# Kernel optimization log

Hardware: AMD Instinct MI355X
Metric: run time of the kernel (lower is better)

The kernel has to match this reference:

```python
import jax, jax.numpy as jnp
import numpy as np
from jax import lax

EPS = 1e-6


def _layernorm(x, g, b, eps=1e-5):
    m = x.mean(-1, keepdims=True)
    v = x.var(-1, keepdims=True)
    return (x - m) / jnp.sqrt(v + eps) * g + b


def _causal_conv(x, w, b, dilation):
    # x: [B,S,D], w: [K, D_in, D_out] -> causal (left) padded dilated conv + GELU, residual
    k = w.shape[0]
    pad = (k - 1) * dilation
    y = lax.conv_general_dilated(
        x, w, window_strides=(1,), padding=[(pad, 0)], rhs_dilation=(dilation,),
        dimension_numbers=('NWC', 'WIO', 'NWC'))
    return x + jax.nn.gelu(y + b)


def setup_inputs() -> dict:
    key = jax.random.key(0)
    B, S, D, DC, N_LTM, K_WM, KS = 4, 2048, 1024, 256, 768, 8, 5
    ks = jax.random.split(key, 24)
    sc = 0.02

    def n(k, shape, scale=sc):
        return jax.random.normal(k, shape, jnp.float32) * scale

    return {
        'x': jax.random.normal(ks[0], (B, S, D), jnp.float32),
        'cache': jax.random.normal(ks[1], (B, N_LTM, DC), jnp.float32),
        'wm': jax.random.normal(ks[2], (B, K_WM, DC + 1), jnp.float32),
        # LTM read projections
        'Wq_ltm': n(ks[3], (D, DC)), 'Wo_ltm': n(ks[4], (DC, D)), 'wg_ltm': n(ks[5], (D,)),
        # WM read projections
        'Wq_wm': n(ks[6], (D, DC)), 'Wo_wm': n(ks[7], (DC, D)), 'wg_wm': n(ks[8], (D,)),
        # causal dilated conv stack (2 layers, k=5, dilations 1 and 2)
        'conv1_w': n(ks[9], (KS, D, D)), 'conv1_b': jnp.zeros((D,), jnp.float32),
        'conv2_w': n(ks[10], (KS, D, D)), 'conv2_b': jnp.zeros((D,), jnp.float32),
        'ln_g': jnp.ones((D,), jnp.float32), 'ln_b': jnp.zeros((D,), jnp.float32),
        # WM write (learned slot keys for addressing)
        'Wqw_wm': n(ks[11], (D, DC)), 'Ww_wm': n(ks[12], (D, DC)),
        'wm_keys': n(ks[13], (K_WM, DC), 1.0), 'wgw_wm': n(ks[14], (D,)),
        # LTM write (content-based addressing against cache)
        'Wqw_ltm': n(ks[15], (D, DC)), 'Ww_ltm': n(ks[16], (D, DC)), 'wgw_ltm': n(ks[17], (D,)),
    }


def reference(x, cache, wm, Wq_ltm, Wo_ltm, wg_ltm, Wq_wm, Wo_wm, wg_wm,
              conv1_w, conv1_b, conv2_w, conv2_b, ln_g, ln_b,
              Wqw_wm, Ww_wm, wm_keys, wgw_wm, Wqw_ltm, Ww_ltm, wgw_ltm):
    DC = cache.shape[-1]
    inv_sqrt = 1.0 / jnp.sqrt(jnp.float32(DC))

    # ---- LTM READ: content-addressed soft read, gated residual blend ----
    q = x @ Wq_ltm                                                  # [B,S,DC]
    attn = jax.nn.softmax(jnp.einsum('bsd,bnd->bsn', q, cache) * inv_sqrt, -1)
    read = jnp.einsum('bsn,bnd->bsd', attn, cache)                  # [B,S,DC]
    gate = jax.nn.sigmoid(x @ wg_ltm)[..., None]                    # [B,S,1]
    x_ltm = x + gate * (read @ Wo_ltm)

    # ---- WM READ (read_decay=0.0 -> wm unchanged by read) ----
    content = wm[..., :DC]                                          # [B,Kw,DC]
    q2 = x_ltm @ Wq_wm
    attn2 = jax.nn.softmax(jnp.einsum('bsd,bkd->bsk', q2, content) * inv_sqrt, -1)
    read2 = jnp.einsum('bsk,bkd->bsd', attn2, content)
    gate2 = jax.nn.sigmoid(x_ltm @ wg_wm)[..., None]
    x_enh = x_ltm + gate2 * (read2 @ Wo_wm)

    # ---- COMPUTE: causal dilated conv stack + post-LayerNorm ----
    h = _causal_conv(x_enh, conv1_w, conv1_b, 1)
    h = _causal_conv(h, conv2_w, conv2_b, 2)
    out = _layernorm(h, ln_g, ln_b)                                 # [B,S,D]

    # ---- WM WRITE: gated soft-WTA addressing vs learned slot keys ----
    qw = out @ Wqw_wm                                               # [B,S,DC]
    aw = jax.nn.softmax(jnp.einsum('bsd,kd->bsk', qw, wm_keys) * inv_sqrt, -1)
    gw = jax.nn.sigmoid(out @ wgw_wm)[..., None]                    # [B,S,1]
    w = gw * aw                                                     # [B,S,Kw]
    tot = w.sum(1)                                                  # [B,Kw]
    c = out @ Ww_wm                                                 # [B,S,DC]
    avg = jnp.einsum('bsk,bsd->bkd', w, c) / (tot[..., None] + EPS)
    alpha = jnp.clip(tot, 0.0, 1.0)[..., None]
    new_content = (1.0 - alpha) * content + alpha * avg
    new_valid = jnp.clip(wm[..., DC] + tot, 0.0, 1.0)               # validity channel
    updated_wm = jnp.concatenate([new_content, new_valid[..., None]], -1)

    # ---- LTM WRITE: gated soft blended write, content-addressed vs cache ----
    ql = out @ Wqw_ltm
    al = jax.nn.softmax(jnp.einsum('bsd,bnd->bsn', ql, cache) * inv_sqrt, -1)
    gl = jax.nn.sigmoid(out @ wgw_ltm)[..., None]
    wl = gl * al                                                    # [B,S,N]
    totl = wl.sum(1)                                                # [B,N]
    cl = out @ Ww_ltm
    avgl = jnp.einsum('bsn,bsd->bnd', wl, cl) / (totl[..., None] + EPS)
    alphal = jnp.clip(totl, 0.0, 1.0)[..., None]
    updated_cache = (1.0 - alphal) * cache + alphal * avgl

    return (out, updated_cache, updated_wm)
```

## Files before the change

### kernel.cpp

```cpp
#include <hip/hip_runtime.h>
#include <stdint.h>

typedef unsigned short u16;
typedef unsigned int u32;
typedef __attribute__((ext_vector_type(8))) short s16x8;
typedef __attribute__((ext_vector_type(4))) float f32x4;

__device__ __forceinline__ float bf2f(u16 u) {
    return __builtin_bit_cast(float, (u32)u << 16);
}
__device__ __forceinline__ u16 f2bf(float f) {
    u32 u = __builtin_bit_cast(u32, f);
    u += 0x7FFFu + ((u >> 16) & 1u);
    return (u16)(u >> 16);
}

__device__ __forceinline__ void gl16(const u16* g, u16* l) {
    __builtin_amdgcn_global_load_lds(
        (const __attribute__((address_space(1))) u32*)(const void*)g,
        (__attribute__((address_space(3))) u32*)(void*)l, 16, 0, 0);
}

#define BAR() { __builtin_amdgcn_sched_barrier(0); __builtin_amdgcn_s_barrier(); __builtin_amdgcn_sched_barrier(0); }

template<int DIL>
__global__ __launch_bounds__(512) void conv8_k(
    const u16* __restrict__ Apad, const u16* __restrict__ Bw,
    float* __restrict__ Cf, float* __restrict__ Cf2)
{
    __shared__ u16 sA[2][16384];
    __shared__ u16 sB[2][16384];
    const int tid  = threadIdx.x;
    const int wid  = tid >> 6;
    const int lane = tid & 63;
    const int wr = (wid >> 2) * 128;
    const int wc = (wid & 3) * 64;
    const int lr = lane & 15;
    const int kq = lane >> 4;
    const int batch = blockIdx.x >> 3;
    const int m0b   = (blockIdx.x & 7) * 256;
    const int bn0   = blockIdx.y * 256;
    const int kbeg  = blockIdx.z * 2560;
    const u16* Ab = Apad + (long)batch * 2056 * 1024;

    const int row0 = tid >> 3;
    const int g0   = (tid & 7) ^ (row0 & 7);

    f32x4 acc[8][4] = {};
    s16x8 aF[4][2], bF[4][2];

    auto stageA = [&](int nb, int kt, int h) {
        const int ktabs = kbeg + kt * 64;
        const int tap = ktabs >> 10;
        const long rbase = (long)(8 + m0b + h * 128 + (tap - 4) * DIL) * 1024
                           + (ktabs & 1023) + g0 * 8;
        u16* dst = &sA[nb][h * 8192 + tid * 8];
        gl16(Ab + rbase + (long)row0 * 1024, dst);
        gl16(Ab + rbase + (long)(row0 + 64) * 1024, dst + 4096);
    };
    auto stageB = [&](int nb, int kt, int h) {
        const int ktabs = kbeg + kt * 64;
        const long rbase = (long)(bn0 + h * 128) * 5120 + ktabs + g0 * 8;
        u16* dst = &sB[nb][h * 8192 + tid * 8];
        gl16(Bw + rbase + (long)row0 * 5120, dst);
        gl16(Bw + rbase + (long)(row0 + 64) * 5120, dst + 4096);
    };
    auto readA = [&](int nb, int mq) {
        #pragma unroll
        for (int m = 0; m < 4; m++) {
            const int row = wr + (mq * 4 + m) * 16 + lr;
            #pragma unroll
            for (int ks = 0; ks < 2; ks++) {
                const int chunk = ks * 4 + kq;
                aF[m][ks] = *(const s16x8*)&sA[nb][row * 64 + ((chunk ^ (row & 7)) << 3)];
            }
        }
    };
    auto readB4 = [&](int nb, int nq) {
        #pragma unroll
        for (int n = 0; n < 2; n++) {
            const int row = wc + (nq * 2 + n) * 16 + lr;
            #pragma unroll
            for (int ks = 0; ks < 2; ks++) {
                const int chunk = ks * 4 + kq;
                bF[nq * 2 + n][ks] = *(const s16x8*)&sB[nb][row * 64 + ((chunk ^ (row & 7)) << 3)];
            }
        }
    };

#define MFQ(MQ, NQ) \
    { __builtin_amdgcn_s_setprio(1); \
      _Pragma("unroll") \
      for (int m = 0; m < 4; m++) { \
        _Pragma("unroll") \
        for (int n = 0; n < 2; n++) { \
          _Pragma("unroll") \
          for (int ks = 0; ks < 2; ks++) \
            acc[(MQ)*4+m][(NQ)*2+n] = __builtin_amdgcn_mfma_f32_16x16x32_bf16( \
                aF[m][ks], bF[(NQ)*2+n][ks], acc[(MQ)*4+m][(NQ)*2+n], 0, 0, 0); \
        } } \
      __builtin_amdgcn_s_setprio(0); }

    stageB(0, 0, 0); stageB(0, 0, 1); stageA(0, 0, 0); stageA(0, 0, 1);

    const int NT = 40;
    for (int t = 0; t < NT; ++t) {
        const int nb = t & 1;
        asm volatile("s_waitcnt vmcnt(4)" ::: "memory");
        BAR();
        readB4(nb, 0); readB4(nb, 1);
        if (t + 1 < NT) { stageB(nb ^ 1, t + 1, 0); stageB(nb ^ 1, t + 1, 1); }
        if (t + 1 < NT) { asm volatile("s_waitcnt vmcnt(4)" ::: "memory"); }
        else            { asm volatile("s_waitcnt vmcnt(0)" ::: "memory"); }
        BAR();
        readA(nb, 0);
        MFQ(0, 0); MFQ(0, 1);
        if (t + 1 < NT) { stageA(nb ^ 1, t + 1, 0); stageA(nb ^ 1, t + 1, 1); }
        readA(nb, 1);
        MFQ(1, 0); MFQ(1, 1);
    }
#undef MFQ

    float* C = (blockIdx.z ? Cf2 : Cf) + (long)batch * 2048 * 1024;
    #pragma unroll
    for (int m = 0; m < 8; m++) {
        #pragma unroll
        for (int n = 0; n < 4; n++) {
            const int cc = bn0 + wc + n * 16 + lr;
            #pragma unroll
            for (int j = 0; j < 4; j++) {
                const int r = m0b + wr + m * 16 + kq * 4 + j;
                C[(long)r * 1024 + cc] = acc[m][n][j];
            }
        }
    }
}

template<int AL, int BL, int EPI, int TN, int KS, int SWZ>
__global__ __launch_bounds__(256) void gemm_bf16(
    const u16* __restrict__ A, const u16* __restrict__ B,
    float* __restrict__ Cf, u16* __restrict__ Cb,
    const float* __restrict__ res, const float* __restrict__ gate,
    int M, int N, int K, int lda, int ldb,
    long aBS, long bBS, long cBS,
    float* __restrict__ Pp, long pStride, int nby)
{
    constexpr int NFRAG = TN / 32;
    __shared__ u16 sA[128 * 32];
    __shared__ u16 sB[TN * 32];
    const int tid  = threadIdx.x;
    const int lane = tid & 63;
    const int wave = tid >> 6;
    const int wr = (wave >> 1) * 64;
    const int wc = (wave & 1) * (TN / 2);

    int bidx, bidy;
    if (SWZ) {
        const int nb  = gridDim.x;
        const int cpx = nb >> 3;
        const int bf  = blockIdx.x;
        const int sw  = (bf & 7) * cpx + (bf >> 3);
        bidx = sw / nby; bidy = sw - bidx * nby;
    } else {
        bidx = blockIdx.x; bidy = blockIdx.y;
    }
    const int m0 = bidx * 128;
    const int n0 = bidy * TN;
    const int zz = blockIdx.z;
    const long bz = (KS > 1) ? (zz / KS) : zz;
    const int ks  = (KS > 1) ? (zz % KS) : 0;
    const u16* Ab = A + bz * aBS;
    const u16* Bb = B + bz * bBS;

    f32x4 acc[4][NFRAG] = {};
    const int lr = lane & 15;
    const int lk = (lane >> 4) << 3;
    const int ar0 = tid >> 2;
    const int akg = (tid & 3) << 3;

    const int Kp = K / KS;
    const int kbeg = ks * Kp, kend = kbeg + Kp;

    for (int kk = kbeg; kk < kend; kk += 32) {
        __syncthreads();
        if (AL == 0) {
            gl16(Ab + (long)(m0 + ar0) * lda + kk + akg,      sA + tid * 8);
            gl16(Ab + (long)(m0 + ar0 + 64) * lda + kk + akg, sA + tid * 8 + 2048);
        } else {
            for (int t = tid; t < 512; t += 256) {
                int row = t & 127, kg = (t >> 7) << 3;
                u32 w0[4];
                #pragma unroll
                for (int j2 = 0; j2 < 4; j2++) {
                    u16 lo = Ab[(long)(kk + kg + 2*j2    ) * lda + m0 + row];
                    u16 hi = Ab[(long)(kk + kg + 2*j2 + 1) * lda + m0 + row];
                    w0[j2] = (u32)lo | ((u32)hi << 16);
                }
                uint4 v; v.x = w0[0]; v.y = w0[1]; v.z = w0[2]; v.w = w0[3];
                *reinterpret_cast<uint4*>(sA + row * 32 + kg) = v;
            }
        }
        if (BL == 1) {
            gl16(Bb + (long)(n0 + ar0) * ldb + kk + akg, sB + tid * 8);
            if (TN == 128)
                gl16(Bb + (long)(n0 + ar0 + 64) * ldb + kk + akg, sB + tid * 8 + 2048);
        } else {
            for (int t = tid; t < TN * 4; t += 256) {
                int col = t & (TN - 1), kg = (t / TN) << 3;
                u32 w0[4];
                #pragma unroll
                for (int j2 = 0; j2 < 4; j2++) {
                    u16 lo = Bb[(long)(kk + kg + 2*j2    ) * ldb + n0 + col];
                    u16 hi = Bb[(long)(kk + kg + 2*j2 + 1) * ldb + n0 + col];
                    w0[j2] = (u32)lo | ((u32)hi << 16);
                }
                uint4 v; v.x = w0[0]; v.y = w0[1]; v.z = w0[2]; v.w = w0[3];
                *reinterpret_cast<uint4*>(sB + col * 32 + kg) = v;
            }
        }
        __syncthreads();
        s16x8 aF[4], bF[NFRAG];
        #pragma unroll
        for (int m = 0; m < 4; m++)
            aF[m] = *reinterpret_cast<const s16x8*>(sA + (wr + m*16 + lr) * 32 + lk);
        #pragma unroll
        for (int n = 0; n < NFRAG; n++)
            bF[n] = *reinterpret_cast<const s16x8*>(sB + (wc + n*16 + lr) * 32 + lk);
        #pragma unroll
        for (int m = 0; m < 4; m++)
            #pragma unroll
            for (int n = 0; n < NFRAG; n++)
                acc[m][n] = __builtin_amdgcn_mfma_f32_16x16x32_bf16(aF[m], bF[n], acc[m][n], 0, 0, 0);
    }

    const int rj = (lane >> 4) << 2;
    if (KS > 1) {
        float* Pb = Pp + (long)ks * pStride + bz * cBS;
        #pragma unroll
        for (int m = 0; m < 4; m++)
            #pragma unroll
            for (int n = 0; n < NFRAG; n++) {
                const int cc = n0 + wc + n*16 + lr;
                #pragma unroll
                for (int j = 0; j < 4; j++) {
                    const int r = m0 + wr + m*16 + rj + j;
                    Pb[(long)r * N + cc] = acc[m][n][j];
                }
            }
        return;
    }

    float* Cfb = Cf + bz * cBS;
    #pragma unroll
    for (int m = 0; m < 4; m++) {
        #pragma unroll
        for (int n = 0; n < NFRAG; n++) {
            const int cc = n0 + wc + n*16 + lr;
            #pragma unroll
            for (int j = 0; j < 4; j++) {
                const int r = m0 + wr + m*16 + rj + j;
                const long idx = (long)r * N + cc;
                const float v = acc[m][n][j];
                if (EPI == 0) {
                    Cb[bz * cBS + idx] = f2bf(v);
                } else if (EPI == 1) {
                    Cfb[idx] = v;
                } else {
                    float o = res[idx] + gate[r] * v;
                    Cfb[idx] = o;
                    if (EPI == 2) Cb[idx] = f2bf(o);
                }
            }
        }
    }
}

template<int KS, int BF>
__global__ __launch_bounds__(256) void ksum_k(
    const float* __restrict__ Pp, long pStride,
    float* __restrict__ outf, u16* __restrict__ outb, int n4)
{
    int i = blockIdx.x * 256 + threadIdx.x;
    if (i >= n4) return;
    float4 s = reinterpret_cast<const float4*>(Pp)[i];
    #pragma unroll
    for (int k = 1; k < KS; k++) {
        float4 v = reinterpret_cast<const float4*>(Pp + (long)k * pStride)[i];
        s.x += v.x; s.y += v.y; s.z += v.z; s.w += v.w;
    }
    if (BF) {
        u32 lo = (u32)f2bf(s.x) | ((u32)f2bf(s.y) << 16);
        u32 hi = (u32)f2bf(s.z) | ((u32)f2bf(s.w) << 16);
        reinterpret_cast<uint2*>(outb)[i] = make_uint2(lo, hi);
    } else {
        reinterpret_cast<float4*>(outf)[i] = s;
    }
}

__global__ void zero_init_k(u16* __restrict__ a, u16* __restrict__ b,
                            float* __restrict__ tot, float* __restrict__ totl)
{
    int i = blockIdx.x * 256 + threadIdx.x;
    int bt = i >> 12, j = i & 4095;
    long off = (long)bt * (2056L * 1024 / 2) + j;
    reinterpret_cast<u32*>(a)[off] = 0u;
    reinterpret_cast<u32*>(b)[off] = 0u;
    if (i < 32) tot[i] = 0.f;
    if (i < 3072) totl[i] = 0.f;
}

__global__ void f32_to_bf16_k(const float* __restrict__ in, u16* __restrict__ out, int n4)
{
    int i = blockIdx.x * 256 + threadIdx.x;
    if (i < n4) {
        float4 v = reinterpret_cast<const float4*>(in)[i];
        u32 lo = (u32)f2bf(v.x) | ((u32)f2bf(v.y) << 16);
        u32 hi = (u32)f2bf(v.z) | ((u32)f2bf(v.w) << 16);
        reinterpret_cast<uint2*>(out)[i] = make_uint2(lo, hi);
    }
}

__global__ __launch_bounds__(256) void transpose_f32_bf16(
    const float* __restrict__ in, u16* __restrict__ out, int R, int C)
{
    __shared__ float tile[32][33];
    long zo = (long)blockIdx.z * R * C;
    in += zo; out += zo;
    int c0 = blockIdx.x * 32, r0 = blockIdx.y * 32;
    int tx = threadIdx.x & 31, ty = threadIdx.x >> 5;
    #pragma unroll
    for (int i = 0; i < 32; i += 8)
        tile[ty + i][tx] = in[(long)(r0 + ty + i) * C + c0 + tx];
    __syncthreads();
    #pragma unroll
    for (int i = 0; i < 32; i += 8)
        out[(long)(c0 + ty + i) * R + r0 + tx] = f2bf(tile[tx][ty + i]);
}

__global__ __launch_bounds__(256) void cw_k(
    const float* __restrict__ wm, const float* __restrict__ Wo, float* __restrict__ CW)
{
    int blk = blockIdx.x;
    const float* wrow = wm + (long)(blk >> 3) * 2056 + (blk & 7) * 257;
    int c = threadIdx.x;
    float a0 = 0.f, a1 = 0.f, a2 = 0.f, a3 = 0.f;
    for (int dd = 0; dd < 256; dd++) {
        float w = wrow[dd];
        const float* wo = Wo + (long)dd * 1024;
        a0 += w * wo[c]; a1 += w * wo[c + 256];
        a2 += w * wo[c + 512]; a3 += w * wo[c + 768];
    }
    float* o = CW + (long)blk * 1024;
    o[c] = a0; o[c + 256] = a1; o[c + 512] = a2; o[c + 768] = a3;
}

__global__ __launch_bounds__(256) void wc_k(
    const float* __restrict__ wm, const u16* __restrict__ WqWt, float* __restrict__ WC)
{
    int blk = blockIdx.x;
    const float* wrow = wm + (long)(blk >> 3) * 2056 + (blk & 7) * 257;
    int c = threadIdx.x;
    float a0 = 0.f, a1 = 0.f, a2 = 0.f, a3 = 0.f;
    for (int j = 0; j < 256; j++) {
        float w = wrow[j];
        const u16* wq = WqWt + (long)j * 1024;
        a0 += bf2f(wq[c])       * w;
        a1 += bf2f(wq[c + 256]) * w;
        a2 += bf2f(wq[c + 512]) * w;
        a3 += bf2f(wq[c + 768]) * w;
    }
    float* o = WC + (long)blk * 1024;
    o[c] = a0; o[c + 256] = a1; o[c + 512] = a2; o[c + 768] = a3;
}

__global__ __launch_bounds__(256) void gemv_sigmoid_k(
    const float* __restrict__ X, const float* __restrict__ w,
    float* __restrict__ out)
{
    int row  = blockIdx.x * 4 + (threadIdx.x >> 6);
    int lane = threadIdx.x & 63;
    const float* xr = X + (long)row * 1024;
    float s = 0.f;
    for (int i = lane; i < 1024; i += 64) s += xr[i] * w[i];
    #pragma unroll
    for (int o = 32; o > 0; o >>= 1) s += __shfl_down(s, o);
    if (lane == 0) out[row] = 1.f / (1.f + __expf(-s));
}

__global__ __launch_bounds__(256) void gemv_sigmoid2_k(
    const float* __restrict__ X, const float* __restrict__ w1, const float* __restrict__ w2,
    float* __restrict__ o1, float* __restrict__ o2)
{
    int row  = blockIdx.x * 4 + (threadIdx.x >> 6);
    int lane = threadIdx.x & 63;
    const float* xr = X + (long)row * 1024;
    float s1 = 0.f, s2 = 0.f;
    for (int i = lane; i < 1024; i += 64) {
        float xv = xr[i];
        s1 += xv * w1[i]; s2 += xv * w2[i];
    }
    #pragma unroll
    for (int o = 32; o > 0; o >>= 1) { s1 += __shfl_down(s1, o); s2 += __shfl_down(s2, o); }
    if (lane == 0) {
        o1[row] = 1.f / (1.f + __expf(-s1));
        o2[row] = 1.f / (1.f + __expf(-s2));
    }
}

__global__ __launch_bounds__(256) void softmax768_k(
    const float* __restrict__ scores, u16* __restrict__ out,
    const float* __restrict__ gate)
{
    __shared__ float s4[4], s4b[4];
    int row = blockIdx.x;
    int t = threadIdx.x;
    const float* sr = scores + (long)row * 768;
    float v[3];
    float m = -1e30f;
    #pragma unroll
    for (int i = 0; i < 3; i++) { v[i] = sr[t + i*256] * 0.0625f; m = fmaxf(m, v[i]); }
    float wm_ = m;
    #pragma unroll
    for (int o = 32; o > 0; o >>= 1) wm_ = fmaxf(wm_, __shfl_down(wm_, o));
    if ((t & 63) == 0) s4[t >> 6] = wm_;
    __syncthreads();
    float bm = fmaxf(fmaxf(s4[0], s4[1]), fmaxf(s4[2], s4[3]));
    float sum = 0.f;
    #pragma unroll
    for (int i = 0; i < 3; i++) { v[i] = __expf(v[i] - bm); sum += v[i]; }
    #pragma unroll
    for (int o = 32; o > 0; o >>= 1) sum += __shfl_down(sum, o);
    if ((t & 63) == 0) s4b[t >> 6] = sum;
    __syncthreads();
    float bs = s4b[0] + s4b[1] + s4b[2] + s4b[3];
    float g = gate ? gate[row] : 1.0f;
    float inv = g / bs;
    u16* orow = out + (long)row * 768;
    #pragma unroll
    for (int i = 0; i < 3; i++) orow[t + i*256] = f2bf(v[i] * inv);
}

__global__ __launch_bounds__(256) void wm_read_fused_k(
    const float* __restrict__ WC, const float* __restrict__ CW,
    const float* __restrict__ gate, const float* __restrict__ res,
    float* __restrict__ outf, u16* __restrict__ outb)
{
    __shared__ float sred[8][4];
    __shared__ float sa[8];
    int row = blockIdx.x;
    int b = row >> 11;
    int d = threadIdx.x, lane = d & 63, wave = d >> 6;
    long orow = (long)row * 1024;
    float rv0 = res[orow + d];
    float rv1 = res[orow + d + 256];
    float rv2 = res[orow + d + 512];
    float rv3 = res[orow + d + 768];
    const float* wcb = WC + (long)b * 8192;
    #pragma unroll
    for (int k = 0; k < 8; k++) {
        const float* w = wcb + k * 1024;
        float v = rv0 * w[d] + rv1 * w[d + 256] + rv2 * w[d + 512] + rv3 * w[d + 768];
        #pragma unroll
        for (int o = 32; o > 0; o >>= 1) v += __shfl_down(v, o);
        if (lane == 0) sred[k][wave] = v;
    }
    __syncthreads();
    if (d < 8) sa[d] = (sred[d][0] + sred[d][1] + sred[d][2] + sred[d][3]) * 0.0625f;
    __syncthreads();
    float m = sa[0];
    #pragma unroll
    for (int k = 1; k < 8; k++) m = fmaxf(m, sa[k]);
    float e[8], sum = 0.f;
    #pragma unroll
    for (int k = 0; k < 8; k++) { e[k] = __expf(sa[k] - m); sum += e[k]; }
    float inv = 1.f / sum;
    #pragma unroll
    for (int k = 0; k < 8; k++) e[k] *= inv;
    float g = gate[row];
    const float* cwb = CW + (long)b * 8192;
    long prow = ((long)(row >> 11) * 2056 + 8 + (row & 2047)) * 1024;
    float rv[4] = { rv0, rv1, rv2, rv3 };
    #pragma unroll
    for (int j = 0; j < 4; j++) {
        int c = d + j * 256;
        float acc = 0.f;
        #pragma unroll
        for (int k = 0; k < 8; k++) acc += e[k] * cwb[k * 1024 + c];
        float o = rv[j] + g * acc;
        outf[orow + c] = o;
        outb[prow + c] = f2bf(o);
    }
}

template<int PAD>
__global__ __launch_bounds__(256) void gelu_reduce_k(
    const float4* p0, const float4* p1, const float4* res,
    const float* __restrict__ bias, float4* outf, u16* outb)
{
    int i4 = blockIdx.x * 256 + threadIdx.x;
    int r = i4 >> 8, c4 = (i4 & 255) << 2;
    float4 a = p0[i4], b = p1[i4], rr = res[i4];
    float4 bi = *reinterpret_cast<const float4*>(bias + c4);
    float o[4];
    float y0 = a.x + b.x + bi.x, y1 = a.y + b.y + bi.y;
    float y2 = a.z + b.z + bi.z, y3 = a.w + b.w + bi.w;
    const float C0 = 0.79788456080286535588f, C1 = 0.044715f;
    o[0] = rr.x + 0.5f * y0 * (1.f + tanhf(C0 * (y0 + C1 * y0 * y0 * y0)));
    o[1] = rr.y + 0.5f * y1 * (1.f + tanhf(C0 * (y1 + C1 * y1 * y1 * y1)));
    o[2] = rr.z + 0.5f * y2 * (1.f + tanhf(C0 * (y2 + C1 * y2 * y2 * y2)));
    o[3] = rr.w + 0.5f * y3 * (1.f + tanhf(C0 * (y3 + C1 * y3 * y3 * y3)));
    float4 ov; ov.x = o[0]; ov.y = o[1]; ov.z = o[2]; ov.w = o[3];
    outf[i4] = ov;
    if (PAD) {
        long prow = ((long)(r >> 11) * 2056 + 8 + (r & 2047)) * 1024 + c4;
        u32 lo = (u32)f2bf(o[0]) | ((u32)f2bf(o[1]) << 16);
        u32 hi = (u32)f2bf(o[2]) | ((u32)f2bf(o[3]) << 16);
        *reinterpret_cast<uint2*>(outb + prow) = make_uint2(lo, hi);
    }
}

__global__ __launch_bounds__(256) void gelu_ln_k(
    const float4* __restrict__ p0, const float4* __restrict__ p1,
    const float4* __restrict__ res, const float* __restrict__ bias,
    const float* __restrict__ g, const float* __restrict__ b,
    float* __restrict__ outf, u16* __restrict__ outb)
{
    __shared__ float rs[4], rss[4];
    int row = blockIdx.x, t = threadIdx.x;
    long i4 = (long)row * 256 + t;
    float4 a = p0[i4], pb = p1[i4], rr = res[i4];
    float4 bi = reinterpret_cast<const float4*>(bias)[t];
    const float C0 = 0.79788456080286535588f, C1 = 0.044715f;
    float y0 = a.x + pb.x + bi.x, y1 = a.y + pb.y + bi.y;
    float y2 = a.z + pb.z + bi.z, y3 = a.w + pb.w + bi.w;
    float o0 = rr.x + 0.5f * y0 * (1.f + tanhf(C0 * (y0 + C1 * y0 * y0 * y0)));
    float o1 = rr.y + 0.5f * y1 * (1.f + tanhf(C0 * (y1 + C1 * y1 * y1 * y1)));
    float o2 = rr.z + 0.5f * y2 * (1.f + tanhf(C0 * (y2 + C1 * y2 * y2 * y2)));
    float o3 = rr.w + 0.5f * y3 * (1.f + tanhf(C0 * (y3 + C1 * y3 * y3 * y3)));
    float s  = o0 + o1 + o2 + o3;
    float ss = o0*o0 + o1*o1 + o2*o2 + o3*o3;
    #pragma unroll
    for (int o = 32; o > 0; o >>= 1) { s += __shfl_down(s, o); ss += __shfl_down(ss, o); }
    if ((t & 63) == 0) { rs[t >> 6] = s; rss[t >> 6] = ss; }
    __syncthreads();
    float S = rs[0]+rs[1]+rs[2]+rs[3];
    float SS = rss[0]+rss[1]+rss[2]+rss[3];
    float mean = S * (1.f/1024.f);
    float var  = SS * (1.f/1024.f) - mean*mean;
    float rstd = rsqrtf(var + 1e-5f);
    float4 gg = reinterpret_cast<const float4*>(g)[t];
    float4 bv = reinterpret_cast<const float4*>(b)[t];
    float4 y;
    y.x = (o0-mean)*rstd*gg.x + bv.x;
    y.y = (o1-mean)*rstd*gg.y + bv.y;
    y.z = (o2-mean)*rstd*gg.z + bv.z;
    y.w = (o3-mean)*rstd*gg.w + bv.w;
    reinterpret_cast<float4*>(outf)[i4] = y;
    u32 lo = (u32)f2bf(y.x) | ((u32)f2bf(y.y) << 16);
    u32 hi = (u32)f2bf(y.z) | ((u32)f2bf(y.w) << 16);
    reinterpret_cast<uint2*>(outb)[i4] = make_uint2(lo, hi);
}

__global__ __launch_bounds__(256) void attn8_w_k(
    const u16* __restrict__ q, int ldq, const u16* __restrict__ keys,
    const float* __restrict__ gate, float* __restrict__ w_out)
{
    __shared__ float sred[8][4];
    __shared__ float sa[8];
    int row = blockIdx.x;
    int d = threadIdx.x, lane = d & 63, wave = d >> 6;
    float qv = bf2f(q[(long)row * ldq + d]);
    #pragma unroll
    for (int k = 0; k < 8; k++) {
        float v = qv * bf2f(keys[k * 256 + d]);
        #pragma unroll
        for (int o = 32; o > 0; o >>= 1) v += __shfl_down(v, o);
        if (lane == 0) sred[k][wave] = v;
    }
    __syncthreads();
    if (d < 8) sa[d] = (sred[d][0] + sred[d][1] + sred[d][2] + sred[d][3]) * 0.0625f;
    __syncthreads();
    if (d < 8) {
        float m = sa[0];
        #pragma unroll
        for (int k = 1; k < 8; k++) m = fmaxf(m, sa[k]);
        float e = __expf(sa[d] - m), sum = 0.f;
        #pragma unroll
        for (int k = 0; k < 8; k++) sum += __expf(sa[k] - m);
        w_out[(long)row * 8 + d] = gate[row] * e / sum;
    }
}

__global__ __launch_bounds__(256) void tot8_k(const float* __restrict__ wD, float* __restrict__ tot)
{
    __shared__ float s4[4];
    int b = blockIdx.y;
    int s = blockIdx.x * 256 + threadIdx.x;
    const float* p = wD + ((long)b * 2048 + s) * 8;
    float v[8];
    #pragma unroll
    for (int k = 0; k < 8; k++) v[k] = p[k];
    for (int k = 0; k < 8; k++) {
        float xv = v[k];
        #pragma unroll
        for (int o = 32; o > 0; o >>= 1) xv += __shfl_down(xv, o);
        if ((threadIdx.x & 63) == 0) s4[threadIdx.x >> 6] = xv;
        __syncthreads();
        if (threadIdx.x == 0) atomicAdd(&tot[b*8 + k], s4[0]+s4[1]+s4[2]+s4[3]);
        __syncthreads();
    }
}

__global__ __launch_bounds__(256) void wm_avg_partial_k(
    const float* __restrict__ wD, const u16* __restrict__ cw, float* __restrict__ part)
{
    int blk = blockIdx.x;
    int b = blk >> 6, k = (blk >> 3) & 7, ch = blk & 7;
    int d = threadIdx.x;
    const float* wp = wD + ((long)b * 2048 + ch * 256) * 8 + k;
    const u16*   cp = cw + ((long)b * 2048 + ch * 256) * 1024 + 256 + d;
    float acc = 0.f;
    for (int s = 0; s < 256; s++) acc += wp[s * 8] * bf2f(cp[(long)s * 1024]);
    part[(long)blk * 256 + d] = acc;
}

__global__ __launch_bounds__(256) void wm_final_k(
    const float* __restrict__ part, const float* __restrict__ wm,
    const float* __restrict__ tot, float* __restrict__ out)
{
    int bk = blockIdx.x;
    int d = threadIdx.x;
    float acc = 0.f;
    #pragma unroll
    for (int ch = 0; ch < 8; ch++) acc += part[((long)bk * 8 + ch) * 256 + d];
    float t = tot[bk];
    float alpha = fminf(fmaxf(t, 0.f), 1.f);
    float avg = acc / (t + 1e-6f);
    long base = (long)(bk >> 3) * 2056 + (bk & 7) * 257;
    out[base + d] = (1.f - alpha) * wm[base + d] + alpha * avg;
    if (d == 0) out[base + 256] = fminf(fmaxf(wm[base + 256] + t, 0.f), 1.f);
}

__global__ void colsum_wl_k(const u16* __restrict__ wl, float* __restrict__ totl)
{
    int b = blockIdx.z;
    int n = blockIdx.x * 256 + threadIdx.x;
    int s0 = blockIdx.y * 256;
    const u16* p = wl + ((long)b * 2048 + s0) * 768 + n;
    float acc = 0.f;
    for (int s = 0; s < 256; s++) acc += bf2f(p[(long)s * 768]);
    atomicAdd(&totl[b * 768 + n], acc);
}

__global__ void cache_blend_k(const float* __restrict__ cache, const float* __restrict__ Sg,
                              const float* __restrict__ totl, float* __restrict__ out)
{
    long i = (long)blockIdx.x * 256 + threadIdx.x;
    int bn = (int)(i >> 8);
    float t = totl[bn];
    float a = fminf(fmaxf(t, 0.f), 1.f);
    out[i] = (1.f - a) * cache[i] + a * (Sg[i] / (t + 1e-6f));
}

extern "C" void kernel_launch(void* const* d_in, const int* in_sizes, int n_in,
                              void* d_out, int out_size, void* d_ws, size_t ws_size,
                              hipStream_t stream)
{
    const int D = 1024, DC = 256, NL = 768;
    const long MS = 8192;
    const long SB = 2048;

    const float* x       = (const float*)d_in[0];
    const float* cache   = (const float*)d_in[1];
    const float* wm      = (const float*)d_in[2];
    const float* Wq_ltm  = (const float*)d_in[3];
    const float* Wo_ltm  = (const float*)d_in[4];
    const float* wg_ltm  = (const float*)d_in[5];
    const float* Wq_wm   = (const float*)d_in[6];
    const float* Wo_wm   = (const float*)d_in[7];
    const float* wg_wm   = (const float*)d_in[8];
    const float* conv1_w = (const float*)d_in[9];
    const float* conv1_b = (const float*)d_in[10];
    const float* conv2_w = (const float*)d_in[11];
    const float* conv2_b = (const float*)d_in[12];
    const float* ln_g    = (const float*)d_in[13];
    const float* ln_b    = (const float*)d_in[14];
    const float* Wqw_wm  = (const float*)d_in[15];
    const float* Ww_wm   = (const float*)d_in[16];
    const float* wm_keys = (const float*)d_in[17];
    const float* wgw_wm  = (const float*)d_in[18];
    const float* Wqw_ltm = (const float*)d_in[19];
    const float* Ww_ltm  = (const float*)d_in[20];
    const float* wgw_ltm = (const float*)d_in[21];

    float* out_f     = (float*)d_out;
    float* cache_out = out_f + 8388608;
    float* wm_out    = out_f + 8388608 + 786432;

    char* ws = (char*)d_ws;
    size_t off = 0;
    auto alloc = [&](size_t bytes) -> char* {
        char* p = ws + off;
        off = (off + bytes + 255) & ~(size_t)255;
        return p;
    };
    u16* WqLt    = (u16*)alloc((size_t)D*DC*2);
    u16* WoLt    = (u16*)alloc((size_t)D*DC*2);
    u16* WqWt    = (u16*)alloc((size_t)D*DC*2);
    u16* WbigT   = (u16*)alloc((size_t)D*D*2);
    u16* c1wt    = (u16*)alloc((size_t)5*D*D*2);
    u16* c2wt    = (u16*)alloc((size_t)5*D*D*2);
    u16* cache_b = (u16*)alloc((size_t)4*NL*DC*2);
    u16* cache_t = (u16*)alloc((size_t)4*NL*DC*2);
    u16* keys_b  = (u16*)alloc((size_t)8*DC*2);
    u16* act0    = (u16*)alloc((size_t)MS*D*2);
    u16* act1    = (u16*)alloc((size_t)MS*D*2);
    u16* xpad1   = (u16*)alloc((size_t)4*2056*1024*2);
    u16* xpad2   = (u16*)alloc((size_t)4*2056*1024*2);
    u16* qb      = (u16*)alloc((size_t)MS*DC*2);
    u16* attnb   = (u16*)alloc((size_t)MS*NL*2);
    u16* readb   = (u16*)alloc((size_t)MS*DC*2);
    float* fact0 = (float*)alloc((size_t)MS*D*4);
    float* fact1 = (float*)alloc((size_t)MS*D*4);
    float* P     = (float*)alloc((size_t)MS*D*4);
    float* CW    = (float*)alloc((size_t)4*8*D*4);
    float* WC    = (float*)alloc((size_t)4*8*D*4);
    float* gateb = (float*)alloc((size_t)MS*4);
    float* gateb2= (float*)alloc((size_t)MS*4);
    float* wD    = (float*)alloc((size_t)MS*8*4);
    float* tot   = (float*)alloc((size_t)4*8*4);
    float* totl  = (float*)alloc((size_t)4*NL*4);
    float* part  = (float*)alloc((size_t)256*256*4);
    float* avglS = (float*)alloc((size_t)4*NL*DC*4);
    float* scores = fact0;
    u16*   qbig   = act0;

    auto cv = [&](const float* in, u16* out, long n) {
        long n4 = n / 4;
        f32_to_bf16_k<<<dim3((unsigned)((n4 + 255) / 256)), 256, 0, stream>>>(in, out, (int)n4);
    };
    auto tr = [&](const float* in, u16* out, int R, int C, int Z) {
        transpose_f32_bf16<<<dim3(C/32, R/32, Z), 256, 0, stream>>>(in, out, R, C);
    };

    zero_init_k<<<64, 256, 0, stream>>>(xpad1, xpad2, tot, totl);
    cv(x, act0, MS * D);
    cv(cache, cache_b, (long)4 * NL * DC);
    cv(wm_keys, keys_b, 8 * DC);
    tr(Wq_ltm,  WqLt,  D, DC, 1);
    tr(Wo_ltm,  WoLt,  DC, D, 1);
    tr(Wq_wm,   WqWt,  D, DC, 1);
    tr(Wqw_wm,  WbigT + 0*256*1024, D, DC, 1);
    tr(Ww_wm,   WbigT + 1*256*1024, D, DC, 1);
    tr(Wqw_ltm, WbigT + 2*256*1024, D, DC, 1);
    tr(Ww_ltm,  WbigT + 3*256*1024, D, DC, 1);
    tr(conv1_w, c1wt, 5*D, D, 1);
    tr(conv2_w, c2wt, 5*D, D, 1);
    tr(cache,   cache_t, NL, DC, 4);
    cw_k<<<32, 256, 0, stream>>>(wm, Wo_wm, CW);
    wc_k<<<32, 256, 0, stream>>>(wm, WqWt, WC);

    gemm_bf16<0,1,0,64,4,1><<<dim3(256,1,4), 256, 0, stream>>>(
        act0, WqLt, nullptr, nullptr, nullptr, nullptr,
        8192,256,1024,1024,1024, 0,0,0, P, 2097152L, 4);
    ksum_k<4,1><<<2048, 256, 0, stream>>>(P, 2097152L, nullptr, qb, 524288);
    gemv_sigmoid_k<<<2048, 256, 0, stream>>>(x, wg_ltm, gateb);
    gemm_bf16<0,1,1,128,1,1><<<dim3(96,1,4), 256, 0, stream>>>(
        qb, cache_b, scores, nullptr, nullptr, nullptr,
        2048,768,256,256,256, SB*256, (long)NL*DC, SB*768, nullptr, 0, 6);
    softmax768_k<<<8192, 256, 0, stream>>>(scores, attnb, nullptr);
    gemm_bf16<0,1,0,64,2,1><<<dim3(64,1,8), 256, 0, stream>>>(
        attnb, cache_t, nullptr, nullptr, nullptr, nullptr,
        2048,256,768,768,768, SB*768, (long)NL*DC, SB*256, P, 2097152L, 4);
    ksum_k<2,1><<<2048, 256, 0, stream>>>(P, 2097152L, nullptr, readb, 524288);
    gemm_bf16<0,1,5,128,1,1><<<dim3(512,1,1), 256, 0, stream>>>(
        readb, WoLt, fact0, nullptr, x, gateb,
        8192,1024,256,256,256, 0,0,0, nullptr, 0, 8);

    gemv_sigmoid_k<<<2048, 256, 0, stream>>>(fact0, wg_wm, gateb);
    wm_read_fused_k<<<8192, 256, 0, stream>>>(WC, CW, gateb, fact0, fact1, xpad1);

    conv8_k<1><<<dim3(32,4,2), 512, 0, stream>>>(xpad1, c1wt, fact0, P);
    gelu_reduce_k<1><<<8192, 256, 0, stream>>>(
        (const float4*)fact0, (const float4*)P, (const float4*)fact1,
        conv1_b, (float4*)fact0, xpad2);
    conv8_k<2><<<dim3(32,4,2), 512, 0, stream>>>(xpad2, c2wt, fact1, P);
    gelu_ln_k<<<8192, 256, 0, stream>>>(
        (const float4*)fact1, (const float4*)P, (const float4*)fact0,
        conv2_b, ln_g, ln_b, out_f, act1);

    gemm_bf16<0,1,0,128,1,1><<<dim3(512,1,1), 256, 0, stream>>>(
        act1, WbigT, nullptr, qbig, nullptr, nullptr,
        8192,1024,1024,1024,1024, 0,0,0, nullptr, 0, 8);
    gemv_sigmoid2_k<<<2048, 256, 0, stream>>>(out_f, wgw_wm, wgw_ltm, gateb, gateb2);
    attn8_w_k<<<8192, 256, 0, stream>>>(qbig, 1024, keys_b, gateb, wD);
    tot8_k<<<dim3(8, 4), 256, 0, stream>>>(wD, tot);
    wm_avg_partial_k<<<256, 256, 0, stream>>>(wD, qbig, part);
    wm_final_k<<<32, 256, 0, stream>>>(part, wm, tot, wm_out);

    gemm_bf16<0,1,1,128,1,1><<<dim3(96,1,4), 256, 0, stream>>>(
        qbig + 512, cache_b, scores, nullptr, nullptr, nullptr,
        2048,768,256,1024,256, SB*1024, (long)NL*DC, SB*768, nullptr, 0, 6);
    softmax768_k<<<8192, 256, 0, stream>>>(scores, attnb, gateb2);
    colsum_wl_k<<<dim3(3, 8, 4), 256, 0, stream>>>(attnb, totl);
    gemm_bf16<1,0,1,64,4,0><<<dim3(6,4,16), 256, 0, stream>>>(
        attnb, qbig + 768, nullptr, nullptr, nullptr, nullptr,
        768,256,2048,768,1024, SB*768, SB*1024, 196608L, P, 786432L, 0);
    ksum_k<4,0><<<768, 256, 0, stream>>>(P, 786432L, avglS, nullptr, 196608);
    cache_blend_k<<<3072, 256, 0, stream>>>(cache, avglS, totl, cache_out);

    (void)in_sizes; (void)n_in; (void)out_size; (void)ws_size;
}
```

Before: 577.0 us.

## Store split-K partials in bf16, merge transposes, fuse gate gemvs, swizzle conv grid

Split-K partial buffers for the conv and GEMM kernels are now written and read as bf16 instead of fp32, which halves the partial-sum traffic. All weight and cache transposes move into one launch, and the sigmoid gate gemvs are folded into the WM read and WM attention kernels. The conv grid is flattened with a block swizzle meant to improve L2 locality. Rounding partials to bf16 before summing loses accuracy in the conv outputs and the sums.

```diff
diff --git a/kernel.cpp b/kernel.cpp
--- a/kernel.cpp
+++ b/kernel.cpp
@@ -14,6 +14,10 @@
     u += 0x7FFFu + ((u >> 16) & 1u);
     return (u16)(u >> 16);
 }
+__device__ __forceinline__ void unpk4(uint2 r, float* o) {
+    o[0] = bf2f((u16)(r.x & 0xffff)); o[1] = bf2f((u16)(r.x >> 16));
+    o[2] = bf2f((u16)(r.y & 0xffff)); o[3] = bf2f((u16)(r.y >> 16));
+}
 
 __device__ __forceinline__ void gl16(const u16* g, u16* l) {
     __builtin_amdgcn_global_load_lds(
@@ -26,7 +30,7 @@
 template<int DIL>
 __global__ __launch_bounds__(512) void conv8_k(
     const u16* __restrict__ Apad, const u16* __restrict__ Bw,
-    float* __restrict__ Cf, float* __restrict__ Cf2)
+    u16* __restrict__ Cb0, u16* __restrict__ Cb1)
 {
     __shared__ u16 sA[2][16384];
     __shared__ u16 sB[2][16384];
@@ -37,10 +41,13 @@
     const int wc = (wid & 3) * 64;
     const int lr = lane & 15;
     const int kq = lane >> 4;
-    const int batch = blockIdx.x >> 3;
-    const int m0b   = (blockIdx.x & 7) * 256;
-    const int bn0   = blockIdx.y * 256;
-    const int kbeg  = blockIdx.z * 2560;
+    const int sw = (blockIdx.x & 7) * 32 + (blockIdx.x >> 3);
+    const int z    = sw >> 7;
+    const int bn0  = ((sw >> 5) & 3) * 256;
+    const int xm   = sw & 31;
+    const int batch = xm >> 3;
+    const int m0b   = (xm & 7) * 256;
+    const int kbeg  = z * 2560;
     const u16* Ab = Apad + (long)batch * 2056 * 1024;
 
     const int row0 = tid >> 3;
@@ -121,7 +128,7 @@
     }
 #undef MFQ
 
-    float* C = (blockIdx.z ? Cf2 : Cf) + (long)batch * 2048 * 1024;
+    u16* C = (z ? Cb1 : Cb0) + (long)batch * 2048 * 1024;
     #pragma unroll
     for (int m = 0; m < 8; m++) {
         #pragma unroll
@@ -130,7 +137,7 @@
             #pragma unroll
             for (int j = 0; j < 4; j++) {
                 const int r = m0b + wr + m * 16 + kq * 4 + j;
-                C[(long)r * 1024 + cc] = acc[m][n][j];
+                C[(long)r * 1024 + cc] = f2bf(acc[m][n][j]);
             }
         }
     }
@@ -143,7 +150,7 @@
     const float* __restrict__ res, const float* __restrict__ gate,
     int M, int N, int K, int lda, int ldb,
     long aBS, long bBS, long cBS,
-    float* __restrict__ Pp, long pStride, int nby)
+    u16* __restrict__ Pp, long pStride, int nby)
 {
     constexpr int NFRAG = TN / 32;
     __shared__ u16 sA[128 * 32];
@@ -235,7 +242,7 @@
 
     const int rj = (lane >> 4) << 2;
     if (KS > 1) {
-        float* Pb = Pp + (long)ks * pStride + bz * cBS;
+        u16* Pb = Pp + (long)ks * pStride + bz * cBS;
         #pragma unroll
         for (int m = 0; m < 4; m++)
             #pragma unroll
@@ -244,7 +251,7 @@
                 #pragma unroll
                 for (int j = 0; j < 4; j++) {
                     const int r = m0 + wr + m*16 + rj + j;
-                    Pb[(long)r * N + cc] = acc[m][n][j];
+                    Pb[(long)r * N + cc] = f2bf(acc[m][n][j]);
                 }
             }
         return;
@@ -277,23 +284,25 @@
 
 template<int KS, int BF>
 __global__ __launch_bounds__(256) void ksum_k(
-    const float* __restrict__ Pp, long pStride,
+    const u16* __restrict__ Pp, long pStride,
     float* __restrict__ outf, u16* __restrict__ outb, int n4)
 {
     int i = blockIdx.x * 256 + threadIdx.x;
     if (i >= n4) return;
-    float4 s = reinterpret_cast<const float4*>(Pp)[i];
-    #pragma unroll
-    for (int k = 1; k < KS; k++) {
-        float4 v = reinterpret_cast<const float4*>(Pp + (long)k * pStride)[i];
-        s.x += v.x; s.y += v.y; s.z += v.z; s.w += v.w;
+    float s[4] = {0.f, 0.f, 0.f, 0.f};
+    #pragma unroll
+    for (int k = 0; k < KS; k++) {
+        uint2 r = reinterpret_cast<const uint2*>(Pp + (long)k * pStride)[i];
+        float v[4]; unpk4(r, v);
+        s[0] += v[0]; s[1] += v[1]; s[2] += v[2]; s[3] += v[3];
     }
     if (BF) {
-        u32 lo = (u32)f2bf(s.x) | ((u32)f2bf(s.y) << 16);
-        u32 hi = (u32)f2bf(s.z) | ((u32)f2bf(s.w) << 16);
+        u32 lo = (u32)f2bf(s[0]) | ((u32)f2bf(s[1]) << 16);
+        u32 hi = (u32)f2bf(s[2]) | ((u32)f2bf(s[3]) << 16);
         reinterpret_cast<uint2*>(outb)[i] = make_uint2(lo, hi);
     } else {
-        reinterpret_cast<float4*>(outf)[i] = s;
+        float4 o; o.x = s[0]; o.y = s[1]; o.z = s[2]; o.w = s[3];
+        reinterpret_cast<float4*>(outf)[i] = o;
     }
 }
 
@@ -320,13 +329,42 @@
     }
 }
 
-__global__ __launch_bounds__(256) void transpose_f32_bf16(
-    const float* __restrict__ in, u16* __restrict__ out, int R, int C)
-{
+__global__ __launch_bounds__(256) void tr_all_k(
+    const float* __restrict__ Wq_ltm, const float* __restrict__ Wq_wm,
+    const float* __restrict__ Wqw_wm, const float* __restrict__ Ww_wm,
+    const float* __restrict__ Wqw_ltm, const float* __restrict__ Ww_ltm,
+    const float* __restrict__ Wo_ltm, const float* __restrict__ conv1_w,
+    const float* __restrict__ conv2_w, const float* __restrict__ cache,
+    u16* __restrict__ WqLt, u16* __restrict__ WqWt, u16* __restrict__ WbigT,
+    u16* __restrict__ WoLt, u16* __restrict__ c1wt, u16* __restrict__ c2wt,
+    u16* __restrict__ cache_t)
+{
+    int b = blockIdx.x;
+    const float* in; u16* out; int R, C, l;
+    if (b < 1536) {
+        l = b & 255; R = 1024; C = 256;
+        int m = b >> 8;
+        if      (m == 0) { in = Wq_ltm;  out = WqLt; }
+        else if (m == 1) { in = Wq_wm;   out = WqWt; }
+        else if (m == 2) { in = Wqw_wm;  out = WbigT; }
+        else if (m == 3) { in = Ww_wm;   out = WbigT + 262144; }
+        else if (m == 4) { in = Wqw_ltm; out = WbigT + 524288; }
+        else             { in = Ww_ltm;  out = WbigT + 786432; }
+    } else if (b < 1792) {
+        l = b - 1536; in = Wo_ltm; out = WoLt; R = 256; C = 1024;
+    } else if (b < 6912) {
+        l = b - 1792; in = conv1_w; out = c1wt; R = 5120; C = 1024;
+    } else if (b < 12032) {
+        l = b - 6912; in = conv2_w; out = c2wt; R = 5120; C = 1024;
+    } else {
+        int lb = b - 12032;
+        int z = lb / 192; l = lb % 192;
+        in = cache + (long)z * 196608; out = cache_t + (long)z * 196608;
+        R = 768; C = 256;
+    }
+    const int ct = C >> 5;
+    const int c0 = (l % ct) * 32, r0 = (l / ct) * 32;
     __shared__ float tile[32][33];
-    long zo = (long)blockIdx.z * R * C;
-    in += zo; out += zo;
-    int c0 = blockIdx.x * 32, r0 = blockIdx.y * 32;
     int tx = threadIdx.x & 31, ty = threadIdx.x >> 5;
     #pragma unroll
     for (int i = 0; i < 32; i += 8)
@@ -387,26 +425,6 @@
     if (lane == 0) out[row] = 1.f / (1.f + __expf(-s));
 }
 
-__global__ __launch_bounds__(256) void gemv_sigmoid2_k(
-    const float* __restrict__ X, const float* __restrict__ w1, const float* __restrict__ w2,
-    float* __restrict__ o1, float* __restrict__ o2)
-{
-    int row  = blockIdx.x * 4 + (threadIdx.x >> 6);
-    int lane = threadIdx.x & 63;
-    const float* xr = X + (long)row * 1024;
-    float s1 = 0.f, s2 = 0.f;
-    for (int i = lane; i < 1024; i += 64) {
-        float xv = xr[i];
-        s1 += xv * w1[i]; s2 += xv * w2[i];
-    }
-    #pragma unroll
-    for (int o = 32; o > 0; o >>= 1) { s1 += __shfl_down(s1, o); s2 += __shfl_down(s2, o); }
-    if (lane == 0) {
-        o1[row] = 1.f / (1.f + __expf(-s1));
-        o2[row] = 1.f / (1.f + __expf(-s2));
-    }
-}
-
 __global__ __launch_bounds__(256) void softmax768_k(
     const float* __restrict__ scores, u16* __restrict__ out,
     const float* __restrict__ gate)
@@ -442,11 +460,13 @@
 
 __global__ __launch_bounds__(256) void wm_read_fused_k(
     const float* __restrict__ WC, const float* __restrict__ CW,
-    const float* __restrict__ gate, const float* __restrict__ res,
+    const float* __restrict__ wg, const float* __restrict__ res,
     float* __restrict__ outf, u16* __restrict__ outb)
 {
     __shared__ float sred[8][4];
+    __shared__ float sg4[4];
     __shared__ float sa[8];
+    __shared__ float gsh;
     int row = blockIdx.x;
     int b = row >> 11;
     int d = threadIdx.x, lane = d & 63, wave = d >> 6;
@@ -455,6 +475,10 @@
     float rv1 = res[orow + d + 256];
     float rv2 = res[orow + d + 512];
     float rv3 = res[orow + d + 768];
+    float gp = rv0 * wg[d] + rv1 * wg[d + 256] + rv2 * wg[d + 512] + rv3 * wg[d + 768];
+    #pragma unroll
+    for (int o = 32; o > 0; o >>= 1) gp += __shfl_down(gp, o);
+    if (lane == 0) sg4[wave] = gp;
     const float* wcb = WC + (long)b * 8192;
     #pragma unroll
     for (int k = 0; k < 8; k++) {
@@ -466,6 +490,7 @@
     }
     __syncthreads();
     if (d < 8) sa[d] = (sred[d][0] + sred[d][1] + sred[d][2] + sred[d][3]) * 0.0625f;
+    if (d == 0) gsh = 1.f / (1.f + __expf(-(sg4[0] + sg4[1] + sg4[2] + sg4[3])));
     __syncthreads();
     float m = sa[0];
     #pragma unroll
@@ -476,7 +501,7 @@
     float inv = 1.f / sum;
     #pragma unroll
     for (int k = 0; k < 8; k++) e[k] *= inv;
-    float g = gate[row];
+    float g = gsh;
     const float* cwb = CW + (long)b * 8192;
     long prow = ((long)(row >> 11) * 2056 + 8 + (row & 2047)) * 1024;
     float rv[4] = { rv0, rv1, rv2, rv3 };
@@ -494,16 +519,19 @@
 
 template<int PAD>
 __global__ __launch_bounds__(256) void gelu_reduce_k(
-    const float4* p0, const float4* p1, const float4* res,
-    const float* __restrict__ bias, float4* outf, u16* outb)
+    const u16* __restrict__ p0, const u16* __restrict__ p1, const float4* __restrict__ res,
+    const float* __restrict__ bias, float4* __restrict__ outf, u16* __restrict__ outb)
 {
     int i4 = blockIdx.x * 256 + threadIdx.x;
     int r = i4 >> 8, c4 = (i4 & 255) << 2;
-    float4 a = p0[i4], b = p1[i4], rr = res[i4];
+    float a[4], b[4];
+    unpk4(reinterpret_cast<const uint2*>(p0)[i4], a);
+    unpk4(reinterpret_cast<const uint2*>(p1)[i4], b);
+    float4 rr = res[i4];
     float4 bi = *reinterpret_cast<const float4*>(bias + c4);
     float o[4];
-    float y0 = a.x + b.x + bi.x, y1 = a.y + b.y + bi.y;
-    float y2 = a.z + b.z + bi.z, y3 = a.w + b.w + bi.w;
+    float y0 = a[0] + b[0] + bi.x, y1 = a[1] + b[1] + bi.y;
+    float y2 = a[2] + b[2] + bi.z, y3 = a[3] + b[3] + bi.w;
     const float C0 = 0.79788456080286535588f, C1 = 0.044715f;
     o[0] = rr.x + 0.5f * y0 * (1.f + tanhf(C0 * (y0 + C1 * y0 * y0 * y0)));
     o[1] = rr.y + 0.5f * y1 * (1.f + tanhf(C0 * (y1 + C1 * y1 * y1 * y1)));
@@ -520,7 +548,7 @@
 }
 
 __global__ __launch_bounds__(256) void gelu_ln_k(
-    const float4* __restrict__ p0, const float4* __restrict__ p1,
+    const u16* __restrict__ p0, const u16* __restrict__ p1,
     const float4* __restrict__ res, const float* __restrict__ bias,
     const float* __restrict__ g, const float* __restrict__ b,
     float* __restrict__ outf, u16* __restrict__ outb)
@@ -528,11 +556,14 @@
     __shared__ float rs[4], rss[4];
     int row = blockIdx.x, t = threadIdx.x;
     long i4 = (long)row * 256 + t;
-    float4 a = p0[i4], pb = p1[i4], rr = res[i4];
+    float a[4], pb[4];
+    unpk4(reinterpret_cast<const uint2*>(p0)[i4], a);
+    unpk4(reinterpret_cast<const uint2*>(p1)[i4], pb);
+    float4 rr = res[i4];
     float4 bi = reinterpret_cast<const float4*>(bias)[t];
     const float C0 = 0.79788456080286535588f, C1 = 0.044715f;
-    float y0 = a.x + pb.x + bi.x, y1 = a.y + pb.y + bi.y;
-    float y2 = a.z + pb.z + bi.z, y3 = a.w + pb.w + bi.w;
+    float y0 = a[0] + pb[0] + bi.x, y1 = a[1] + pb[1] + bi.y;
+    float y2 = a[2] + pb[2] + bi.z, y3 = a[3] + pb[3] + bi.w;
     float o0 = rr.x + 0.5f * y0 * (1.f + tanhf(C0 * (y0 + C1 * y0 * y0 * y0)));
     float o1 = rr.y + 0.5f * y1 * (1.f + tanhf(C0 * (y1 + C1 * y1 * y1 * y1)));
     float o2 = rr.z + 0.5f * y2 * (1.f + tanhf(C0 * (y2 + C1 * y2 * y2 * y2)));
@@ -561,15 +592,27 @@
     reinterpret_cast<uint2*>(outb)[i4] = make_uint2(lo, hi);
 }
 
-__global__ __launch_bounds__(256) void attn8_w_k(
-    const u16* __restrict__ q, int ldq, const u16* __restrict__ keys,
-    const float* __restrict__ gate, float* __restrict__ w_out)
+__global__ __launch_bounds__(256) void attn8_wg_k(
+    const u16* __restrict__ q, const float* __restrict__ xo,
+    const float* __restrict__ w1, const float* __restrict__ w2,
+    const u16* __restrict__ keys, float* __restrict__ wD,
+    float* __restrict__ gateb2)
 {
     __shared__ float sred[8][4];
     __shared__ float sa[8];
+    __shared__ float sg1[4], sg2[4];
+    __shared__ float g1sh;
     int row = blockIdx.x;
     int d = threadIdx.x, lane = d & 63, wave = d >> 6;
-    float qv = bf2f(q[(long)row * ldq + d]);
+    float qv = bf2f(q[(long)row * 1024 + d]);
+    float4 xr  = reinterpret_cast<const float4*>(xo + (long)row * 1024)[d];
+    float4 w1v = reinterpret_cast<const float4*>(w1)[d];
+    float4 w2v = reinterpret_cast<const float4*>(w2)[d];
+    float s1 = xr.x*w1v.x + xr.y*w1v.y + xr.z*w1v.z + xr.w*w1v.w;
+    float s2 = xr.x*w2v.x + xr.y*w2v.y + xr.z*w2v.z + xr.w*w2v.w;
+    #pragma unroll
+    for (int o = 32; o > 0; o >>= 1) { s1 += __shfl_down(s1, o); s2 += __shfl_down(s2, o); }
+    if (lane == 0) { sg1[wave] = s1; sg2[wave] = s2; }
     #pragma unroll
     for (int k = 0; k < 8; k++) {
         float v = qv * bf2f(keys[k * 256 + d]);
@@ -579,6 +622,10 @@
     }
     __syncthreads();
     if (d < 8) sa[d] = (sred[d][0] + sred[d][1] + sred[d][2] + sred[d][3]) * 0.0625f;
+    if (d == 0) {
+        g1sh = 1.f / (1.f + __expf(-(sg1[0] + sg1[1] + sg1[2] + sg1[3])));
+        gateb2[row] = 1.f / (1.f + __expf(-(sg2[0] + sg2[1] + sg2[2] + sg2[3])));
+    }
     __syncthreads();
     if (d < 8) {
         float m = sa[0];
@@ -587,7 +634,7 @@
         float e = __expf(sa[d] - m), sum = 0.f;
         #pragma unroll
         for (int k = 0; k < 8; k++) sum += __expf(sa[k] - m);
-        w_out[(long)row * 8 + d] = gate[row] * e / sum;
+        wD[(long)row * 8 + d] = g1sh * e / sum;
     }
 }
 
@@ -722,7 +769,7 @@
     u16* readb   = (u16*)alloc((size_t)MS*DC*2);
     float* fact0 = (float*)alloc((size_t)MS*D*4);
     float* fact1 = (float*)alloc((size_t)MS*D*4);
-    float* P     = (float*)alloc((size_t)MS*D*4);
+    u16* Pu      = (u16*)alloc((size_t)16777216*2);
     float* CW    = (float*)alloc((size_t)4*8*D*4);
     float* WC    = (float*)alloc((size_t)4*8*D*4);
     float* gateb = (float*)alloc((size_t)MS*4);
@@ -739,31 +786,21 @@
         long n4 = n / 4;
         f32_to_bf16_k<<<dim3((unsigned)((n4 + 255) / 256)), 256, 0, stream>>>(in, out, (int)n4);
     };
-    auto tr = [&](const float* in, u16* out, int R, int C, int Z) {
-        transpose_f32_bf16<<<dim3(C/32, R/32, Z), 256, 0, stream>>>(in, out, R, C);
-    };
 
     zero_init_k<<<64, 256, 0, stream>>>(xpad1, xpad2, tot, totl);
     cv(x, act0, MS * D);
     cv(cache, cache_b, (long)4 * NL * DC);
     cv(wm_keys, keys_b, 8 * DC);
-    tr(Wq_ltm,  WqLt,  D, DC, 1);
-    tr(Wo_ltm,  WoLt,  DC, D, 1);
-    tr(Wq_wm,   WqWt,  D, DC, 1);
-    tr(Wqw_wm,  WbigT + 0*256*1024, D, DC, 1);
-    tr(Ww_wm,   WbigT + 1*256*1024, D, DC, 1);
-    tr(Wqw_ltm, WbigT + 2*256*1024, D, DC, 1);
-    tr(Ww_ltm,  WbigT + 3*256*1024, D, DC, 1);
-    tr(conv1_w, c1wt, 5*D, D, 1);
-    tr(conv2_w, c2wt, 5*D, D, 1);
-    tr(cache,   cache_t, NL, DC, 4);
+    tr_all_k<<<12800, 256, 0, stream>>>(
+        Wq_ltm, Wq_wm, Wqw_wm, Ww_wm, Wqw_ltm, Ww_ltm, Wo_ltm, conv1_w, conv2_w, cache,
+        WqLt, WqWt, WbigT, WoLt, c1wt, c2wt, cache_t);
     cw_k<<<32, 256, 0, stream>>>(wm, Wo_wm, CW);
     wc_k<<<32, 256, 0, stream>>>(wm, WqWt, WC);
 
     gemm_bf16<0,1,0,64,4,1><<<dim3(256,1,4), 256, 0, stream>>>(
         act0, WqLt, nullptr, nullptr, nullptr, nullptr,
-        8192,256,1024,1024,1024, 0,0,0, P, 2097152L, 4);
-    ksum_k<4,1><<<2048, 256, 0, stream>>>(P, 2097152L, nullptr, qb, 524288);
+        8192,256,1024,1024,1024, 0,0,0, Pu, 2097152L, 4);
+    ksum_k<4,1><<<2048, 256, 0, stream>>>(Pu, 2097152L, nullptr, qb, 524288);
     gemv_sigmoid_k<<<2048, 256, 0, stream>>>(x, wg_ltm, gateb);
     gemm_bf16<0,1,1,128,1,1><<<dim3(96,1,4), 256, 0, stream>>>(
         qb, cache_b, scores, nullptr, nullptr, nullptr,
@@ -771,29 +808,25 @@
     softmax768_k<<<8192, 256, 0, stream>>>(scores, attnb, nullptr);
     gemm_bf16<0,1,0,64,2,1><<<dim3(64,1,8), 256, 0, stream>>>(
         attnb, cache_t, nullptr, nullptr, nullptr, nullptr,
-        2048,256,768,768,768, SB*768, (long)NL*DC, SB*256, P, 2097152L, 4);
-    ksum_k<2,1><<<2048, 256, 0, stream>>>(P, 2097152L, nullptr, readb, 524288);
+        2048,256,768,768,768, SB*768, (long)NL*DC, SB*256, Pu, 2097152L, 4);
+    ksum_k<2,1><<<2048, 256, 0, stream>>>(Pu, 2097152L, nullptr, readb, 524288);
     gemm_bf16<0,1,5,128,1,1><<<dim3(512,1,1), 256, 0, stream>>>(
         readb, WoLt, fact0, nullptr, x, gateb,
         8192,1024,256,256,256, 0,0,0, nullptr, 0, 8);
 
-    gemv_sigmoid_k<<<2048, 256, 0, stream>>>(fact0, wg_wm, gateb);
-    wm_read_fused_k<<<8192, 256, 0, stream>>>(WC, CW, gateb, fact0, fact1, xpad1);
-
-    conv8_k<1><<<dim3(32,4,2), 512, 0, stream>>>(xpad1, c1wt, fact0, P);
+    wm_read_fused_k<<<8192, 256, 0, stream>>>(WC, CW, wg_wm, fact0, fact1, xpad1);
+
+    conv8_k<1><<<256, 512, 0, stream>>>(xpad1, c1wt, Pu, Pu + 8388608);
     gelu_reduce_k<1><<<8192, 256, 0, stream>>>(
-        (const float4*)fact0, (const float4*)P, (const float4*)fact1,
-        conv1_b, (float4*)fact0, xpad2);
-    conv8_k<2><<<dim3(32,4,2), 512, 0, stream>>>(xpad2, c2wt, fact1, P);
+        Pu, Pu + 8388608, (const float4*)fact1, conv1_b, (float4*)fact0, xpad2);
+    conv8_k<2><<<256, 512, 0, stream>>>(xpad2, c2wt, Pu, Pu + 8388608);
     gelu_ln_k<<<8192, 256, 0, stream>>>(
-        (const float4*)fact1, (const float4*)P, (const float4*)fact0,
-        conv2_b, ln_g, ln_b, out_f, act1);
+        Pu, Pu + 8388608, (const float4*)fact0, conv2_b, ln_g, ln_b, out_f, act1);
 
     gemm_bf16<0,1,0,128,1,1><<<dim3(512,1,1), 256, 0, stream>>>(
         act1, WbigT, nullptr, qbig, nullptr, nullptr,
         8192,1024,1024,1024,1024, 0,0,0, nullptr, 0, 8);
-    gemv_sigmoid2_k<<<2048, 256, 0, stream>>>(out_f, wgw_wm, wgw_ltm, gateb, gateb2);
-    attn8_w_k<<<8192, 256, 0, stream>>>(qbig, 1024, keys_b, gateb, wD);
+    attn8_wg_k<<<8192, 256, 0, stream>>>(qbig, out_f, wgw_wm, wgw_ltm, keys_b, wD, gateb2);
     tot8_k<<<dim3(8, 4), 256, 0, stream>>>(wD, tot);
     wm_avg_partial_k<<<256, 256, 0, stream>>>(wD, qbig, part);
     wm_final_k<<<32, 256, 0, stream>>>(part, wm, tot, wm_out);
@@ -805,8 +838,8 @@
     colsum_wl_k<<<dim3(3, 8, 4), 256, 0, stream>>>(attnb, totl);
     gemm_bf16<1,0,1,64,4,0><<<dim3(6,4,16), 256, 0, stream>>>(
         attnb, qbig + 768, nullptr, nullptr, nullptr, nullptr,
-        768,256,2048,768,1024, SB*768, SB*1024, 196608L, P, 786432L, 0);
-    ksum_k<4,0><<<768, 256, 0, stream>>>(P, 786432L, avglS, nullptr, 196608);
+        768,256,2048,768,1024, SB*768, SB*1024, 196608L, Pu, 786432L, 0);
+    ksum_k<4,0><<<768, 256, 0, stream>>>(Pu, 786432L, avglS, nullptr, 196608);
     cache_blend_k<<<3072, 256, 0, stream>>>(cache, avglS, totl, cache_out);
 
     (void)in_sizes; (void)n_in; (void)out_size; (void)ws_size;
```

Result: faster. 531.0 us (-8.0%).
